# Kernel optimization log

Hardware: AMD Instinct MI355X
Metric: run time of the kernel (lower is better)

Reference implementation:

```python
import jax, jax.numpy as jnp
import numpy as np

NUM_HEADS = 16
THETA = 10000.0


def _rope(x, cos, sin):
    # x: [B, H, S, d_k]; cos/sin: [S, d_k//2]
    x_even = x[..., 0::2]
    x_odd = x[..., 1::2]
    out_even = x_even * cos - x_odd * sin
    out_odd = x_odd * cos + x_even * sin
    # interleave back to original even/odd layout
    return jnp.stack([out_even, out_odd], axis=-1).reshape(x.shape)


def setup_inputs() -> dict:
    key = jax.random.key(0)
    ks = jax.random.split(key, 5)
    B, S, D = 2, 2048, 1024
    std = 2.0 / (D + D)
    return {
        "x": jax.random.normal(ks[0], (B, S, D), dtype=jnp.float32),
        "w_q": jax.random.normal(ks[1], (D, D), dtype=jnp.float32) * std,
        "w_k": jax.random.normal(ks[2], (D, D), dtype=jnp.float32) * std,
        "w_v": jax.random.normal(ks[3], (D, D), dtype=jnp.float32) * std,
        "w_o": jax.random.normal(ks[4], (D, D), dtype=jnp.float32) * std,
    }


def reference(x, w_q, w_k, w_v, w_o):
    B, S, D = x.shape
    H = NUM_HEADS
    d_k = D // H

    # QKV projections: x @ W.T
    q = jnp.einsum('bsd,ed->bse', x, w_q).reshape(B, S, H, d_k).transpose(0, 2, 1, 3)
    k = jnp.einsum('bsd,ed->bse', x, w_k).reshape(B, S, H, d_k).transpose(0, 2, 1, 3)
    v = jnp.einsum('bsd,ed->bse', x, w_v).reshape(B, S, H, d_k).transpose(0, 2, 1, 3)

    # RoPE (token_positions = arange(S))
    pos = jnp.arange(S, dtype=jnp.float32)
    inv_freq = 1.0 / (THETA ** (2.0 * jnp.arange(d_k // 2, dtype=jnp.float32) / d_k))
    angles = pos[:, None] * inv_freq[None, :]  # [S, d_k//2]
    cos, sin = jnp.cos(angles), jnp.sin(angles)
    q = _rope(q, cos, sin)
    k = _rope(k, cos, sin)

    # causal attention
    scores = jnp.einsum('bhqd,bhkd->bhqk', q, k) / jnp.sqrt(jnp.float32(d_k))
    causal = jnp.tril(jnp.ones((S, S), dtype=bool))
    scores = jnp.where(causal[None, None], scores, -jnp.inf)
    attn = jax.nn.softmax(scores, axis=-1)
    out = jnp.einsum('bhqk,bhkd->bhqd', attn, v)  # [B, H, S, d_k]

    out = out.transpose(0, 2, 1, 3).reshape(B, S, D)
    return jnp.einsum('bsd,ed->bse', out, w_o)
```

## Files before the change

kernel.cpp:

```cpp
#include <hip/hip_runtime.h>

typedef unsigned short u16;
typedef unsigned int u32;
typedef short bf16x8 __attribute__((ext_vector_type(8)));
typedef float f32x4 __attribute__((ext_vector_type(4)));

#define CSC 0.18033688011112042f

__device__ __forceinline__ u16 f2bf(float f) {
    union { float f; unsigned u; } x; x.f = f;
    unsigned r = x.u + 0x7fffu + ((x.u >> 16) & 1u);
    return (u16)(r >> 16);
}
__device__ __forceinline__ float bf2f(u16 v) {
    union { unsigned u; float f; } x; x.u = ((unsigned)v) << 16;
    return x.f;
}
__device__ __forceinline__ u32 cvt_pk_bf16(float lo, float hi) {
    u32 r;
    asm("v_cvt_pk_bf16_f32 %0, %1, %2" : "=v"(r) : "v"(lo), "v"(hi));
    return r;
}
__device__ __forceinline__ float exp2_fast(float x) {
#if __has_builtin(__builtin_amdgcn_exp2f)
    return __builtin_amdgcn_exp2f(x);
#else
    return exp2f(x);
#endif
}
__device__ __forceinline__ void gl_lds16(const u16* g, u16* l) {
#if __has_builtin(__builtin_amdgcn_global_load_lds)
    __builtin_amdgcn_global_load_lds(
        (const __attribute__((address_space(1))) unsigned int*)g,
        (__attribute__((address_space(3))) unsigned int*)l, 16, 0, 0);
#else
    *(bf16x8*)l = *(const bf16x8*)g;
#endif
}
__device__ __forceinline__ int ileave(int x) {
    return (x < 16) ? (x << 1) : (((x - 16) << 1) | 1);
}

__global__ void cvt_all_kernel(const float* __restrict__ x, const float* __restrict__ wq,
                               const float* __restrict__ wk, const float* __restrict__ wv,
                               const float* __restrict__ wo,
                               u16* __restrict__ xb, u16* __restrict__ qkvw,
                               u16* __restrict__ ow) {
    int i = blockIdx.x * 256 + threadIdx.x;
    const float4* src;
    ushort4* dst;
    if (i < 1048576) {
        src = (const float4*)x + i;
        dst = (ushort4*)xb + i;
    } else {
        int r = i - 1048576;
        int m = r >> 18;
        int off = r & 262143;
        const float* s4 = (m == 0) ? wq : (m == 1) ? wk : (m == 2) ? wv : wo;
        u16* d = (m < 3) ? (qkvw + (size_t)m * 1048576) : ow;
        src = (const float4*)s4 + off;
        dst = (ushort4*)d + off;
    }
    float4 v = *src;
    ushort4 o;
    o.x = f2bf(v.x); o.y = f2bf(v.y); o.z = f2bf(v.z); o.w = f2bf(v.w);
    *dst = o;
}

__global__ void rope_kernel(u16* __restrict__ qb, u16* __restrict__ kb) {
    int idx = blockIdx.x * 256 + threadIdx.x;
    u16* buf;
    float scale;
    if (blockIdx.y == 0) { buf = qb; scale = CSC; } else { buf = kb; scale = 1.0f; }
    int g   = idx & 7;
    int row = idx >> 3;
    int s   = row & 2047;
    u16* p = buf + (size_t)row * 64 + g * 8;
    bf16x8 v = *(bf16x8*)p;
    bf16x8 o;
    #pragma unroll
    for (int q = 0; q < 4; ++q) {
        int i = g * 4 + q;
        float inv = exp2_fast((float)i * -0.4152410118609203f);
        float ang = (float)s * inv;
        float sn, cs;
        sincosf(ang, &sn, &cs);
        float e  = bf2f(((u16*)&v)[2 * q]);
        float od = bf2f(((u16*)&v)[2 * q + 1]);
        ((u16*)&o)[2 * q]     = f2bf((e * cs - od * sn) * scale);
        ((u16*)&o)[2 * q + 1] = f2bf((od * cs + e * sn) * scale);
    }
    *(bf16x8*)p = o;
}

__global__ __launch_bounds__(256) void gemm_qkv(const u16* __restrict__ A,
                                                const u16* __restrict__ Bw,
                                                u16* __restrict__ C, int K) {
    __shared__ __align__(16) u16 SB[16384];
    u16* SH = SB;
    const int tid  = threadIdx.x;
    const int bm   = blockIdx.x * 128;
    const int bn   = blockIdx.y * 128;
    const int wave = tid >> 6, lane = tid & 63;
    const int wm   = (wave >> 1) * 64, wn = (wave & 1) * 64;
    const int l16  = lane & 15, quad = lane >> 4;
    const int mat  = bn >> 10;

    f32x4 acc[4][4];
    #pragma unroll
    for (int i = 0; i < 4; i++)
        #pragma unroll
        for (int j = 0; j < 4; j++)
            #pragma unroll
            for (int e = 0; e < 4; e++) acc[i][j][e] = 0.0f;

    const int srow = tid >> 2;
    const int scol = (((tid & 3) ^ ((tid >> 3) & 3))) * 8;
    const u16* gA0 = A  + (size_t)(bm + srow) * K + scol;
    const u16* gA1 = A  + (size_t)(bm + 64 + srow) * K + scol;
    const u16* gB0 = Bw + (size_t)(bn + srow) * K + scol;
    const u16* gB1 = Bw + (size_t)(bn + 64 + srow) * K + scol;
    const int csw = (quad ^ ((l16 >> 1) & 3)) * 8;

    auto stage = [&](int k0, int buf) {
        u16* As = SB + buf * 8192;
        u16* Bs = As + 4096;
        gl_lds16(gA0 + k0, As + (size_t)tid * 8);
        gl_lds16(gA1 + k0, As + (size_t)(tid + 256) * 8);
        gl_lds16(gB0 + k0, Bs + (size_t)tid * 8);
        gl_lds16(gB1 + k0, Bs + (size_t)(tid + 256) * 8);
    };

    stage(0, 0);
    int cur = 0;
    for (int k0 = 0; k0 < K; k0 += 32) {
        __syncthreads();
        if (k0 + 32 < K) stage(k0 + 32, cur ^ 1);
        const u16* As = SB + cur * 8192;
        const u16* Bs = As + 4096;
        bf16x8 af[4], bfr[4];
        #pragma unroll
        for (int i = 0; i < 4; i++) af[i]  = *(const bf16x8*)&As[(wm + i * 16 + l16) * 32 + csw];
        #pragma unroll
        for (int j = 0; j < 4; j++) bfr[j] = *(const bf16x8*)&Bs[(wn + j * 16 + l16) * 32 + csw];
        #pragma unroll
        for (int i = 0; i < 4; i++)
            #pragma unroll
            for (int j = 0; j < 4; j++)
                acc[i][j] = __builtin_amdgcn_mfma_f32_16x16x32_bf16(af[i], bfr[j], acc[i][j], 0, 0, 0);
        cur ^= 1;
    }

    const int b  = bm >> 11, sb = bm & 2047;
    if (mat < 2) {
        #pragma unroll
        for (int pass = 0; pass < 2; ++pass) {
            __syncthreads();
            if ((wn >> 6) == pass) {
                #pragma unroll
                for (int i = 0; i < 4; i++)
                    #pragma unroll
                    for (int j = 0; j < 4; j++)
                        #pragma unroll
                        for (int r = 0; r < 4; r++) {
                            int rl = wm + i * 16 + quad * 4 + r;
                            int cl = j * 16 + l16;
                            SH[rl * 66 + cl] = f2bf(acc[i][j][r]);
                        }
            }
            __syncthreads();
            int rl   = tid >> 1;
            int half = (tid & 1) * 32;
            int c    = (bn + pass * 64) & 1023;
            int h    = c >> 6;
            int s    = sb + rl;
            u16* dst = C + (size_t)mat * 4194304 +
                       (((size_t)(b * 16 + h) * 2048 + s) * 64) + half;
            const u16* srcp = &SH[rl * 66 + half];
            #pragma unroll
            for (int kk = 0; kk < 4; ++kk)
                *(bf16x8*)(dst + kk * 8) = *(const bf16x8*)(srcp + kk * 8);
        }
    } else {
        #pragma unroll
        for (int pass = 0; pass < 2; ++pass) {
            __syncthreads();
            if ((wn >> 6) == pass) {
                #pragma unroll
                for (int i = 0; i < 4; i++)
                    #pragma unroll
                    for (int j = 0; j < 4; j++)
                        #pragma unroll
                        for (int r = 0; r < 4; r++) {
                            int row = j * 16 + l16;
                            int ml  = wm + i * 16 + quad * 4 + r;
                            int sp  = (ml & ~31) | ileave(ml & 31);
                            SH[row * 130 + sp] = f2bf(acc[i][j][r]);
                        }
            }
            __syncthreads();
            int row = tid >> 2, seg = tid & 3;
            int cc  = (bn + pass * 64 + row) & 1023;
            int h = cc >> 6, dv = cc & 63;
            u16* dst = C + (size_t)8388608 +
                       (((size_t)(b * 16 + h) * 64 + dv) * 2048) + sb + seg * 32;
            const u16* srcp = &SH[row * 130 + seg * 32];
            #pragma unroll
            for (int kk = 0; kk < 4; ++kk)
                *(bf16x8*)(dst + kk * 8) = *(const bf16x8*)(srcp + kk * 8);
        }
    }
}

__global__ __launch_bounds__(256, 2) void gemm_out(const u16* __restrict__ A,
                                                   const u16* __restrict__ Bw,
                                                   float* __restrict__ C, int K) {
    __shared__ __align__(16) u16 SB[24576];
    const int tid  = threadIdx.x;
    const int bm   = blockIdx.x * 128;
    const int bn   = blockIdx.y * 64;
    const int wave = tid >> 6, lane = tid & 63;
    const int wm   = wave * 32;
    const int l16  = lane & 15, quad = lane >> 4;

    f32x4 acc[2][4];
    #pragma unroll
    for (int i = 0; i < 2; i++)
        #pragma unroll
        for (int j = 0; j < 4; j++)
            #pragma unroll
            for (int e = 0; e < 4; e++) acc[i][j][e] = 0.0f;

    const int srowS = tid >> 3;
    const int scol8 = (((tid & 7) ^ ((tid >> 3) & 7))) * 8;
    const u16* gA = A  + (size_t)(bm + srowS) * K + scol8;
    const u16* gB = Bw + (size_t)(bn + srowS) * K + scol8;
    const int rsw = (l16 & 7);

    auto stage = [&](int k0, int buf) {
        u16* As = SB + buf * 12288;
        u16* Bs = As + 8192;
        #pragma unroll
        for (int l = 0; l < 4; ++l)
            gl_lds16(gA + (size_t)(l * 32) * K + k0, As + (size_t)(l * 256 + tid) * 8);
        #pragma unroll
        for (int l = 0; l < 2; ++l)
            gl_lds16(gB + (size_t)(l * 32) * K + k0, Bs + (size_t)(l * 256 + tid) * 8);
    };

    stage(0, 0);
    int cur = 0;
    for (int k0 = 0; k0 < K; k0 += 64) {
        __syncthreads();
        if (k0 + 64 < K) stage(k0 + 64, cur ^ 1);
        const u16* As = SB + cur * 12288;
        const u16* Bs = As + 8192;
        #pragma unroll
        for (int kk = 0; kk < 2; ++kk) {
            const int ch = ((kk * 4 + quad) ^ rsw) * 8;
            bf16x8 af[2], bfr[4];
            #pragma unroll
            for (int i = 0; i < 2; i++) af[i]  = *(const bf16x8*)&As[(wm + i * 16 + l16) * 64 + ch];
            #pragma unroll
            for (int j = 0; j < 4; j++) bfr[j] = *(const bf16x8*)&Bs[(j * 16 + l16) * 64 + ch];
            #pragma unroll
            for (int i = 0; i < 2; i++)
                #pragma unroll
                for (int j = 0; j < 4; j++)
                    acc[i][j] = __builtin_amdgcn_mfma_f32_16x16x32_bf16(af[i], bfr[j], acc[i][j], 0, 0, 0);
        }
        cur ^= 1;
    }

    __syncthreads();
    float* SHf = (float*)SB;
    #pragma unroll
    for (int i = 0; i < 2; i++)
        #pragma unroll
        for (int j = 0; j < 4; j++)
            #pragma unroll
            for (int r = 0; r < 4; r++)
                SHf[(wm + i * 16 + quad * 4 + r) * 68 + j * 16 + l16] = acc[i][j][r];
    __syncthreads();
    const int rl = tid >> 4;
    const int c4 = (tid & 15) * 4;
    #pragma unroll
    for (int rr = 0; rr < 8; ++rr) {
        int row = rr * 16 + rl;
        float4 v = *(const float4*)&SHf[row * 68 + c4];
        *(float4*)&C[(size_t)(bm + row) * 1024 + bn + c4] = v;
    }
}

__global__ __launch_bounds__(512, 2) void attn_kernel(const u16* __restrict__ Q,
                                                      const u16* __restrict__ Kb,
                                                      const u16* __restrict__ Vt,
                                                      u16* __restrict__ Oout) {
    __shared__ __align__(16) u16 KV[2][8192];
    __shared__ __align__(16) u16 PW[8 * 1024];
    const int tid  = threadIdx.x;
    const int wave = tid >> 6, lane = tid & 63;
    const int side = wave >> 2;
    const int wl   = wave & 3;
    const int l16  = lane & 15, quad = lane >> 4;
    const int bid  = blockIdx.x;
    const int j    = (bid >> 3) & 15;
    const int bh   = (bid & 7) * 4 + (bid >> 7);
    const int T    = 32 - j;
    const int q0   = (side == 0 ? (31 - j) : j) * 64 + wl * 16;
    const int dTil = (side == 0) ? (T - 1) : j;

    const u16* Qh = Q  + (size_t)bh * 2048 * 64;
    const u16* Kh = Kb + (size_t)bh * 2048 * 64;
    const u16* Vh = Vt + (size_t)bh * 64 * 2048;

    bf16x8 qf0 = *(const bf16x8*)&Qh[(size_t)(q0 + l16) * 64 + quad * 8];
    bf16x8 qf1 = *(const bf16x8*)&Qh[(size_t)(q0 + l16) * 64 + 32 + quad * 8];

    f32x4 o[4];
    float ls[4];
    #pragma unroll
    for (int t = 0; t < 4; t++)
        #pragma unroll
        for (int e = 0; e < 4; e++) o[t][e] = 0.0f;
    #pragma unroll
    for (int r = 0; r < 4; r++) ls[r] = 0.0f;

    const int tid2 = tid & 255;
    const int srow = tid2 >> 2;
    const int scs  = (((tid2 & 3) ^ ((tid2 >> 3) & 3))) * 8;
    const u16* gK = Kh + (size_t)srow * 64 + scs;
    const u16* gV = Vh + (size_t)srow * 2048 + scs;

    const int cswz = (quad ^ ((l16 >> 1) & 3)) * 8;
    const int psw0 = ((quad ^ (l16 & 7)) << 3);
    const int psw1 = (((quad ^ (l16 & 7)) ^ 4) << 3);

    u16* pw16 = PW + wave * 1024;
    u32* pw32 = (u32*)pw16;

    auto stage = [&](int t, int buf) {
        u16* base = KV[buf];
        if (tid < 256) {
            gl_lds16(gK + (size_t)t * 4096,      base + (size_t)tid2 * 8);
            gl_lds16(gK + (size_t)t * 4096 + 32, base + 2048 + (size_t)tid2 * 8);
        } else {
            gl_lds16(gV + (size_t)t * 64,        base + 4096 + (size_t)tid2 * 8);
            gl_lds16(gV + (size_t)t * 64 + 32,   base + 6144 + (size_t)tid2 * 8);
        }
    };

    stage(0, 0);
    for (int t = 0; t < T; ++t) {
        __syncthreads();
        if (t + 1 < T) stage(t + 1, (t + 1) & 1);
        const bool act = (side == 0) || (t <= j);
        if (act) {
            const u16* B = KV[t & 1];
            bf16x8 kf0[4], kf1[4], vf0[4], vf1[4];
            #pragma unroll
            for (int n = 0; n < 4; n++) {
                int ri = (n * 16 + l16) * 32 + cswz;
                kf0[n] = *(const bf16x8*)&B[ri];
                kf1[n] = *(const bf16x8*)&B[2048 + ri];
                vf0[n] = *(const bf16x8*)&B[4096 + ri];
                vf1[n] = *(const bf16x8*)&B[6144 + ri];
            }
            const int kbase = t * 64;
            const bool diag = (t == dTil);

            f32x4 s[4];
            __builtin_amdgcn_s_setprio(1);
            #pragma unroll
            for (int n = 0; n < 4; n++) {
                #pragma unroll
                for (int e = 0; e < 4; e++) s[n][e] = 0.0f;
                s[n] = __builtin_amdgcn_mfma_f32_16x16x32_bf16(qf0, kf0[n], s[n], 0, 0, 0);
                s[n] = __builtin_amdgcn_mfma_f32_16x16x32_bf16(qf1, kf1[n], s[n], 0, 0, 0);
            }
            __builtin_amdgcn_s_setprio(0);
            float p[4][4];
            #pragma unroll
            for (int n = 0; n < 4; n++)
                #pragma unroll
                for (int r = 0; r < 4; r++) {
                    float v = exp2_fast(s[n][r]);
                    if (diag) {
                        int row = q0 + quad * 4 + r;
                        v = (kbase + n * 16 + l16 > row) ? 0.0f : v;
                    }
                    p[n][r] = v;
                    ls[r] += v;
                }
            #pragma unroll
            for (int c = 0; c < 2; c++)
                #pragma unroll
                for (int r = 0; r < 4; r++) {
                    int prow = quad * 4 + r;
                    int pj   = (((c * 4 + (l16 >> 2)) ^ (prow & 7)) << 2) | (l16 & 3);
                    pw32[prow * 32 + pj] = cvt_pk_bf16(p[2 * c][r], p[2 * c + 1][r]);
                }
            asm volatile("s_waitcnt lgkmcnt(0)" ::: "memory");
            bf16x8 pf0 = *(const bf16x8*)&pw16[l16 * 64 + psw0];
            bf16x8 pf1 = *(const bf16x8*)&pw16[l16 * 64 + psw1];
            __builtin_amdgcn_s_setprio(1);
            #pragma unroll
            for (int dn = 0; dn < 4; dn++) {
                o[dn] = __builtin_amdgcn_mfma_f32_16x16x32_bf16(pf0, vf0[dn], o[dn], 0, 0, 0);
                o[dn] = __builtin_amdgcn_mfma_f32_16x16x32_bf16(pf1, vf1[dn], o[dn], 0, 0, 0);
            }
            __builtin_amdgcn_s_setprio(0);
        }
    }

    #pragma unroll
    for (int off = 1; off < 16; off <<= 1)
        #pragma unroll
        for (int r = 0; r < 4; r++)
            ls[r] += __shfl_xor(ls[r], off);

    const int b = bh >> 4, h = bh & 15;
    #pragma unroll
    for (int r = 0; r < 4; r++) {
        float inv = 1.0f / ls[r];
        int srw = q0 + quad * 4 + r;
        #pragma unroll
        for (int dn = 0; dn < 4; dn++) {
            int d = h * 64 + dn * 16 + l16;
            Oout[((size_t)b * 2048 + srw) * 1024 + d] = f2bf(o[dn][r] * inv);
        }
    }
}

extern "C" void kernel_launch(void* const* d_in, const int* in_sizes, int n_in,
                              void* d_out, int out_size, void* d_ws, size_t ws_size,
                              hipStream_t stream) {
    const float* x  = (const float*)d_in[0];
    const float* wq = (const float*)d_in[1];
    const float* wk = (const float*)d_in[2];
    const float* wv = (const float*)d_in[3];
    const float* wo = (const float*)d_in[4];
    float* out = (float*)d_out;

    const int M = 4096, D = 1024;
    u16* xb    = (u16*)d_ws;
    u16* qkvw  = xb   + (size_t)M * D;
    u16* ow    = qkvw + (size_t)3 * D * D;
    u16* qkv   = ow   + (size_t)D * D;
    u16* qb    = qkv;
    u16* kb    = qkv + (size_t)M * D;
    u16* vtb   = qkv + (size_t)2 * M * D;
    u16* aob   = qkv + (size_t)3 * M * D;

    cvt_all_kernel<<<8192, 256, 0, stream>>>(x, wq, wk, wv, wo, xb, qkvw, ow);

    dim3 gq(32, 24);
    gemm_qkv<<<gq, 256, 0, stream>>>(xb, qkvw, qkv, D);

    dim3 gr(2048, 2);
    rope_kernel<<<gr, 256, 0, stream>>>(qb, kb);

    attn_kernel<<<512, 512, 0, stream>>>(qb, kb, vtb, aob);

    dim3 go(32, 16);
    gemm_out<<<go, 256, 0, stream>>>(aob, ow, out, D);
}
```

Before: 176.4 us.

## Split long-side key tiles across idle waves to balance causal attention work

In the paired causal attention block, the short-query side's waves used to sit idle once their diagonal was reached. Now they take half of each remaining key tile for the long-query side, splitting the key dimension into two 32-column halves. The partial outputs and row sums are then merged through shared memory at the end. This aims to remove the load imbalance between the two wave groups, at the cost of extra registers for a third accumulator, duplicated V fragment loads and a final reduction pass.

```diff
diff --git a/kernel.cpp b/kernel.cpp
--- a/kernel.cpp
+++ b/kernel.cpp
@@ -307,24 +307,29 @@
     const int j    = (bid >> 3) & 15;
     const int bh   = (bid & 7) * 4 + (bid >> 7);
     const int T    = 32 - j;
-    const int q0   = (side == 0 ? (31 - j) : j) * 64 + wl * 16;
-    const int dTil = (side == 0) ? (T - 1) : j;
+    const int q0A  = j * 64 + wl * 16;
+    const int q0B  = (31 - j) * 64 + wl * 16;
 
     const u16* Qh = Q  + (size_t)bh * 2048 * 64;
     const u16* Kh = Kb + (size_t)bh * 2048 * 64;
     const u16* Vh = Vt + (size_t)bh * 64 * 2048;
 
-    bf16x8 qf0 = *(const bf16x8*)&Qh[(size_t)(q0 + l16) * 64 + quad * 8];
-    bf16x8 qf1 = *(const bf16x8*)&Qh[(size_t)(q0 + l16) * 64 + 32 + quad * 8];
-
-    f32x4 o[4];
-    float ls[4];
+    bf16x8 qBf0 = *(const bf16x8*)&Qh[(size_t)(q0B + l16) * 64 + quad * 8];
+    bf16x8 qBf1 = *(const bf16x8*)&Qh[(size_t)(q0B + l16) * 64 + 32 + quad * 8];
+    bf16x8 qAf0, qAf1;
+    if (side == 1) {
+        qAf0 = *(const bf16x8*)&Qh[(size_t)(q0A + l16) * 64 + quad * 8];
+        qAf1 = *(const bf16x8*)&Qh[(size_t)(q0A + l16) * 64 + 32 + quad * 8];
+    }
+
+    f32x4 oB[4], oA[4], oB2[4];
+    float lsB[4], lsA[4], lsB2[4];
     #pragma unroll
-    for (int t = 0; t < 4; t++)
-        #pragma unroll
-        for (int e = 0; e < 4; e++) o[t][e] = 0.0f;
-    #pragma unroll
-    for (int r = 0; r < 4; r++) ls[r] = 0.0f;
+    for (int t = 0; t < 4; t++) {
+        #pragma unroll
+        for (int e = 0; e < 4; e++) { oB[t][e] = 0.0f; oA[t][e] = 0.0f; oB2[t][e] = 0.0f; }
+        lsB[t] = 0.0f; lsA[t] = 0.0f; lsB2[t] = 0.0f;
+    }
 
     const int tid2 = tid & 255;
     const int srow = tid2 >> 2;
@@ -338,6 +343,8 @@
 
     u16* pw16 = PW + wave * 1024;
     u32* pw32 = (u32*)pw16;
+
+    const u16* Bp = KV[0];
 
     auto stage = [&](int t, int buf) {
         u16* base = KV[buf];
@@ -350,84 +357,183 @@
         }
     };
 
+    auto full_side = [&](const bf16x8& q0f, const bf16x8& q1f, f32x4* o, float* ls,
+                         int q0, int kbase, bool diag) {
+        bf16x8 kf0[4], kf1[4], vf0[4], vf1[4];
+        #pragma unroll
+        for (int n = 0; n < 4; n++) {
+            int ri = (n * 16 + l16) * 32 + cswz;
+            kf0[n] = *(const bf16x8*)&Bp[ri];
+            kf1[n] = *(const bf16x8*)&Bp[2048 + ri];
+            vf0[n] = *(const bf16x8*)&Bp[4096 + ri];
+            vf1[n] = *(const bf16x8*)&Bp[6144 + ri];
+        }
+        f32x4 s[4];
+        __builtin_amdgcn_s_setprio(1);
+        #pragma unroll
+        for (int n = 0; n < 4; n++) {
+            #pragma unroll
+            for (int e = 0; e < 4; e++) s[n][e] = 0.0f;
+            s[n] = __builtin_amdgcn_mfma_f32_16x16x32_bf16(q0f, kf0[n], s[n], 0, 0, 0);
+            s[n] = __builtin_amdgcn_mfma_f32_16x16x32_bf16(q1f, kf1[n], s[n], 0, 0, 0);
+        }
+        __builtin_amdgcn_s_setprio(0);
+        float p[4][4];
+        #pragma unroll
+        for (int n = 0; n < 4; n++)
+            #pragma unroll
+            for (int r = 0; r < 4; r++) {
+                float v = exp2_fast(s[n][r]);
+                if (diag) {
+                    int row = q0 + quad * 4 + r;
+                    v = (kbase + n * 16 + l16 > row) ? 0.0f : v;
+                }
+                p[n][r] = v;
+                ls[r] += v;
+            }
+        #pragma unroll
+        for (int c = 0; c < 2; c++)
+            #pragma unroll
+            for (int r = 0; r < 4; r++) {
+                int prow = quad * 4 + r;
+                int pj   = (((c * 4 + (l16 >> 2)) ^ (prow & 7)) << 2) | (l16 & 3);
+                pw32[prow * 32 + pj] = cvt_pk_bf16(p[2 * c][r], p[2 * c + 1][r]);
+            }
+        asm volatile("s_waitcnt lgkmcnt(0)" ::: "memory");
+        bf16x8 pf0 = *(const bf16x8*)&pw16[l16 * 64 + psw0];
+        bf16x8 pf1 = *(const bf16x8*)&pw16[l16 * 64 + psw1];
+        __builtin_amdgcn_s_setprio(1);
+        #pragma unroll
+        for (int dn = 0; dn < 4; dn++) {
+            o[dn] = __builtin_amdgcn_mfma_f32_16x16x32_bf16(pf0, vf0[dn], o[dn], 0, 0, 0);
+            o[dn] = __builtin_amdgcn_mfma_f32_16x16x32_bf16(pf1, vf1[dn], o[dn], 0, 0, 0);
+        }
+        __builtin_amdgcn_s_setprio(0);
+    };
+
+    auto half_side = [&](const bf16x8& q0f, const bf16x8& q1f, f32x4* o, float* ls,
+                         int q0, int kbase, bool diag, int nbase) {
+        bf16x8 kf0h[2], kf1h[2], vfh[4];
+        #pragma unroll
+        for (int nn = 0; nn < 2; nn++) {
+            int ri = ((nbase + nn) * 16 + l16) * 32 + cswz;
+            kf0h[nn] = *(const bf16x8*)&Bp[ri];
+            kf1h[nn] = *(const bf16x8*)&Bp[2048 + ri];
+        }
+        const int vbase = (nbase == 0) ? 4096 : 6144;
+        #pragma unroll
+        for (int dn = 0; dn < 4; dn++)
+            vfh[dn] = *(const bf16x8*)&Bp[vbase + (dn * 16 + l16) * 32 + cswz];
+        f32x4 s[2];
+        __builtin_amdgcn_s_setprio(1);
+        #pragma unroll
+        for (int nn = 0; nn < 2; nn++) {
+            #pragma unroll
+            for (int e = 0; e < 4; e++) s[nn][e] = 0.0f;
+            s[nn] = __builtin_amdgcn_mfma_f32_16x16x32_bf16(q0f, kf0h[nn], s[nn], 0, 0, 0);
+            s[nn] = __builtin_amdgcn_mfma_f32_16x16x32_bf16(q1f, kf1h[nn], s[nn], 0, 0, 0);
+        }
+        __builtin_amdgcn_s_setprio(0);
+        float p[2][4];
+        #pragma unroll
+        for (int nn = 0; nn < 2; nn++)
+            #pragma unroll
+            for (int r = 0; r < 4; r++) {
+                float v = exp2_fast(s[nn][r]);
+                if (diag) {
+                    int row = q0 + quad * 4 + r;
+                    v = (kbase + (nbase + nn) * 16 + l16 > row) ? 0.0f : v;
+                }
+                p[nn][r] = v;
+                ls[r] += v;
+            }
+        const int c = nbase >> 1;
+        #pragma unroll
+        for (int r = 0; r < 4; r++) {
+            int prow = quad * 4 + r;
+            int pj   = (((c * 4 + (l16 >> 2)) ^ (prow & 7)) << 2) | (l16 & 3);
+            pw32[prow * 32 + pj] = cvt_pk_bf16(p[0][r], p[1][r]);
+        }
+        asm volatile("s_waitcnt lgkmcnt(0)" ::: "memory");
+        const int pswh = (nbase == 0) ? psw0 : psw1;
+        bf16x8 pfh = *(const bf16x8*)&pw16[l16 * 64 + pswh];
+        __builtin_amdgcn_s_setprio(1);
+        #pragma unroll
+        for (int dn = 0; dn < 4; dn++)
+            o[dn] = __builtin_amdgcn_mfma_f32_16x16x32_bf16(pfh, vfh[dn], o[dn], 0, 0, 0);
+        __builtin_amdgcn_s_setprio(0);
+    };
+
     stage(0, 0);
     for (int t = 0; t < T; ++t) {
         __syncthreads();
         if (t + 1 < T) stage(t + 1, (t + 1) & 1);
-        const bool act = (side == 0) || (t <= j);
-        if (act) {
-            const u16* B = KV[t & 1];
-            bf16x8 kf0[4], kf1[4], vf0[4], vf1[4];
-            #pragma unroll
-            for (int n = 0; n < 4; n++) {
-                int ri = (n * 16 + l16) * 32 + cswz;
-                kf0[n] = *(const bf16x8*)&B[ri];
-                kf1[n] = *(const bf16x8*)&B[2048 + ri];
-                vf0[n] = *(const bf16x8*)&B[4096 + ri];
-                vf1[n] = *(const bf16x8*)&B[6144 + ri];
-            }
-            const int kbase = t * 64;
-            const bool diag = (t == dTil);
-
-            f32x4 s[4];
-            __builtin_amdgcn_s_setprio(1);
-            #pragma unroll
-            for (int n = 0; n < 4; n++) {
-                #pragma unroll
-                for (int e = 0; e < 4; e++) s[n][e] = 0.0f;
-                s[n] = __builtin_amdgcn_mfma_f32_16x16x32_bf16(qf0, kf0[n], s[n], 0, 0, 0);
-                s[n] = __builtin_amdgcn_mfma_f32_16x16x32_bf16(qf1, kf1[n], s[n], 0, 0, 0);
-            }
-            __builtin_amdgcn_s_setprio(0);
-            float p[4][4];
-            #pragma unroll
-            for (int n = 0; n < 4; n++)
-                #pragma unroll
-                for (int r = 0; r < 4; r++) {
-                    float v = exp2_fast(s[n][r]);
-                    if (diag) {
-                        int row = q0 + quad * 4 + r;
-                        v = (kbase + n * 16 + l16 > row) ? 0.0f : v;
-                    }
-                    p[n][r] = v;
-                    ls[r] += v;
-                }
-            #pragma unroll
-            for (int c = 0; c < 2; c++)
-                #pragma unroll
-                for (int r = 0; r < 4; r++) {
-                    int prow = quad * 4 + r;
-                    int pj   = (((c * 4 + (l16 >> 2)) ^ (prow & 7)) << 2) | (l16 & 3);
-                    pw32[prow * 32 + pj] = cvt_pk_bf16(p[2 * c][r], p[2 * c + 1][r]);
-                }
-            asm volatile("s_waitcnt lgkmcnt(0)" ::: "memory");
-            bf16x8 pf0 = *(const bf16x8*)&pw16[l16 * 64 + psw0];
-            bf16x8 pf1 = *(const bf16x8*)&pw16[l16 * 64 + psw1];
-            __builtin_amdgcn_s_setprio(1);
+        Bp = KV[t & 1];
+        const int kbase = t * 64;
+        if (t <= j) {
+            if (side == 0) full_side(qBf0, qBf1, oB, lsB, q0B, kbase, t == T - 1);
+            else           full_side(qAf0, qAf1, oA, lsA, q0A, kbase, t == j);
+        } else {
+            if (side == 0) half_side(qBf0, qBf1, oB,  lsB,  q0B, kbase, t == T - 1, 0);
+            else           half_side(qBf0, qBf1, oB2, lsB2, q0B, kbase, t == T - 1, 2);
+        }
+    }
+
+    __syncthreads();
+    float* CB = (float*)&KV[0][0];
+    float* wb = CB + (size_t)wl * 1280;
+    if (side == 1) {
+        #pragma unroll
+        for (int dn = 0; dn < 4; dn++)
+            #pragma unroll
+            for (int e = 0; e < 4; e++)
+                wb[(dn * 4 + e) * 64 + lane] = oB2[dn][e];
+        #pragma unroll
+        for (int r = 0; r < 4; r++)
+            wb[1024 + r * 64 + lane] = lsB2[r];
+    }
+    __syncthreads();
+
+    const int b = bh >> 4, h = bh & 15;
+    if (side == 0) {
+        #pragma unroll
+        for (int dn = 0; dn < 4; dn++)
+            #pragma unroll
+            for (int e = 0; e < 4; e++)
+                oB[dn][e] += wb[(dn * 4 + e) * 64 + lane];
+        #pragma unroll
+        for (int r = 0; r < 4; r++)
+            lsB[r] += wb[1024 + r * 64 + lane];
+        #pragma unroll
+        for (int off = 1; off < 16; off <<= 1)
+            #pragma unroll
+            for (int r = 0; r < 4; r++)
+                lsB[r] += __shfl_xor(lsB[r], off);
+        #pragma unroll
+        for (int r = 0; r < 4; r++) {
+            float inv = 1.0f / lsB[r];
+            int srw = q0B + quad * 4 + r;
             #pragma unroll
             for (int dn = 0; dn < 4; dn++) {
-                o[dn] = __builtin_amdgcn_mfma_f32_16x16x32_bf16(pf0, vf0[dn], o[dn], 0, 0, 0);
-                o[dn] = __builtin_amdgcn_mfma_f32_16x16x32_bf16(pf1, vf1[dn], o[dn], 0, 0, 0);
-            }
-            __builtin_amdgcn_s_setprio(0);
-        }
-    }
-
-    #pragma unroll
-    for (int off = 1; off < 16; off <<= 1)
-        #pragma unroll
-        for (int r = 0; r < 4; r++)
-            ls[r] += __shfl_xor(ls[r], off);
-
-    const int b = bh >> 4, h = bh & 15;
-    #pragma unroll
-    for (int r = 0; r < 4; r++) {
-        float inv = 1.0f / ls[r];
-        int srw = q0 + quad * 4 + r;
-        #pragma unroll
-        for (int dn = 0; dn < 4; dn++) {
-            int d = h * 64 + dn * 16 + l16;
-            Oout[((size_t)b * 2048 + srw) * 1024 + d] = f2bf(o[dn][r] * inv);
+                int d = h * 64 + dn * 16 + l16;
+                Oout[((size_t)b * 2048 + srw) * 1024 + d] = f2bf(oB[dn][r] * inv);
+            }
+        }
+    } else {
+        #pragma unroll
+        for (int off = 1; off < 16; off <<= 1)
+            #pragma unroll
+            for (int r = 0; r < 4; r++)
+                lsA[r] += __shfl_xor(lsA[r], off);
+        #pragma unroll
+        for (int r = 0; r < 4; r++) {
+            float inv = 1.0f / lsA[r];
+            int srw = q0A + quad * 4 + r;
+            #pragma unroll
+            for (int dn = 0; dn < 4; dn++) {
+                int d = h * 64 + dn * 16 + l16;
+                Oout[((size_t)b * 2048 + srw) * 1024 + d] = f2bf(oA[dn][r] * inv);
+            }
         }
     }
 }
```

Result: slower. 195.7 us (+10.9%).
